# Kernel tuning notes

Measured on AMD Instinct MI355X. Metric: run time of the kernel, lower is better.

Reference implementation:

```python
import jax, jax.numpy as jnp
import numpy as np

NT, NGRID, NX, H, NY = 365, 512, 256, 1024, 1
DR = 0.5

def setup_inputs() -> dict:
    key = jax.random.key(0)
    ks = jax.random.split(key, 8)
    s = 1.0 / np.sqrt(H)
    x = jax.random.normal(ks[0], (NT, NGRID, NX), dtype=jnp.float32)
    # variational dropout mask on input: Bernoulli(1-dr)/(1-dr), fixed across timesteps
    keep = 1.0 - DR
    maskX = (jax.random.uniform(ks[1], (NGRID, NX)) < keep).astype(jnp.float32) / keep
    W_ih = jax.random.uniform(ks[2], (4 * H, NX), minval=-s, maxval=s, dtype=jnp.float32)
    W_hh = jax.random.uniform(ks[3], (4 * H, H), minval=-s, maxval=s, dtype=jnp.float32)
    b_ih = jax.random.uniform(ks[4], (4 * H,), minval=-s, maxval=s, dtype=jnp.float32)
    b_hh = jax.random.uniform(ks[5], (4 * H,), minval=-s, maxval=s, dtype=jnp.float32)
    W_lin = jax.random.uniform(ks[6], (NY, H), minval=-s, maxval=s, dtype=jnp.float32)
    b_lin = jax.random.uniform(ks[7], (NY,), minval=-s, maxval=s, dtype=jnp.float32)
    return {"x": x, "maskX": maskX, "W_ih": W_ih, "W_hh": W_hh,
            "b_ih": b_ih, "b_hh": b_hh, "W_lin": W_lin, "b_lin": b_lin}

def reference(x, maskX, W_ih, W_hh, b_ih, b_hh, W_lin, b_lin):
    ngrid = x.shape[1]
    hidden = W_hh.shape[1]
    # dropout mask applied to input at every step (maskH is never used in the original forward)
    xm = x * maskX[None, :, :]                       # [nt, ngrid, nx]
    # precompute input-to-gate projections for all timesteps (one big GEMM)
    gx = jnp.einsum('tbn,gn->tbg', xm, W_ih) + b_ih + b_hh  # [nt, ngrid, 4H]

    def step(carry, gxt):
        h, c = carry
        gates = gxt + h @ W_hh.T                     # [ngrid, 4H]
        i, f, g, o = jnp.split(gates, 4, axis=-1)    # PyTorch LSTMCell gate order
        i = jax.nn.sigmoid(i)
        f = jax.nn.sigmoid(f)
        g = jnp.tanh(g)
        o = jax.nn.sigmoid(o)
        c = f * c + i * g
        h = o * jnp.tanh(c)
        return (h, c), h

    h0 = jnp.zeros((ngrid, hidden), dtype=x.dtype)
    c0 = jnp.zeros((ngrid, hidden), dtype=x.dtype)
    _, hs = jax.lax.scan(step, (h0, c0), gx)          # hs: [nt, ngrid, H]
    out = jnp.einsum('tbh,yh->tby', hs, W_lin) + b_lin
    return out
```

## Files before the change

kernel.cpp:

```cpp
#include <hip/hip_runtime.h>
#include <hip/hip_bf16.h>
#include <stdint.h>

#define NT 365
#define NGRID 512
#define NX 256
#define HID 1024

typedef __bf16 bf16x8 __attribute__((ext_vector_type(8)));
typedef float f32x16 __attribute__((ext_vector_type(16)));
typedef float f32x4  __attribute__((ext_vector_type(4)));
typedef int   i32x4  __attribute__((ext_vector_type(4)));

__device__ __forceinline__ unsigned short f2bf(float f) {
    union { float f; uint32_t u; } v; v.f = f;
    uint32_t u = v.u;
    uint32_t r = (u + 0x7FFFu + ((u >> 16) & 1u)) >> 16;
    return (unsigned short)r;
}
__device__ __forceinline__ float sigmoidf_(float x) {
    return 1.0f / (1.0f + __expf(-x));
}
__device__ __forceinline__ float tanhf_(float x) {
    return 1.0f - 2.0f / (__expf(2.0f * x) + 1.0f);
}
__device__ __forceinline__ f32x16 mfma(bf16x8 a, bf16x8 b, f32x16 c) {
    return __builtin_amdgcn_mfma_f32_32x32x16_bf16(a, b, c, 0, 0, 0);
}


__global__ void pack_w_kernel(const float* __restrict__ W_ih,
                              const float* __restrict__ W_hh,
                              unsigned short* __restrict__ WP) {
    int tid = blockIdx.x * blockDim.x + threadIdx.x;
    if (tid >= 128 * 80 * 64) return;
    int l  = tid & 63;
    int kt = (tid >> 6) % 80;
    int jg = tid / (80 * 64);
    int n = l & 31;
    int gate = n & 3;
    int j = jg * 8 + (n >> 2);
    int k = kt * 16 + ((l >> 5) << 3);
    int row = gate * HID + j;
    const float* src = (k < HID) ? (W_hh + (size_t)row * HID + k)
                                 : (W_ih + (size_t)row * NX + (k - HID));
    unsigned short* dst = WP + (size_t)tid * 8;
    #pragma unroll
    for (int e = 0; e < 8; ++e) dst[e] = f2bf(src[e]);
}

__global__ void pack_xm_kernel(const float* __restrict__ x,
                               const float* __restrict__ maskX,
                               unsigned short* __restrict__ XM) {
    size_t tid = (size_t)blockIdx.x * blockDim.x + threadIdx.x;
    if (tid >= (size_t)NT * 16384) return;
    int l  = tid & 63;
    int a  = (tid >> 6) & 1;
    int kt = (tid >> 7) & 15;
    int bi = (tid >> 11) & 7;
    int t  = tid >> 14;
    int b = bi * 64 + a * 32 + (l & 31);
    int n = kt * 16 + ((l >> 5) << 3);
    const float* xs = x + ((size_t)t * NGRID + b) * NX + n;
    const float* ms = maskX + (size_t)b * NX + n;
    unsigned short* dst = XM + tid * 8;
    #pragma unroll
    for (int e = 0; e < 8; ++e) dst[e] = f2bf(xs[e] * ms[e]);
}

__global__ void init_kernel(float* __restrict__ out,
                            const float* __restrict__ b_lin,
                            int* __restrict__ ctr, int prefill) {
    int i = blockIdx.x * blockDim.x + threadIdx.x;
    if (i < 1024) ctr[i] = 0;
    if (prefill && i < NT * NGRID) out[i] = b_lin[0];
}

__global__ void reduce_out_kernel(const float* __restrict__ OPart,
                                  const float* __restrict__ b_lin,
                                  float* __restrict__ out) {
    int i = blockIdx.x * blockDim.x + threadIdx.x;
    if (i >= NT * NGRID) return;
    int t = i >> 9, b = i & 511;
    int bi = b >> 6, bl = b & 63;
    const float* p = OPart + ((size_t)(t * 8 + bi) * 32) * 64 + bl;
    float s = b_lin[0];
    #pragma unroll
    for (int g = 0; g < 32; ++g) s += p[g * 64];
    out[i] = s;
}

template<bool BAL>
__device__ void lstm_loop(int tid, int bi, int wgJ,
                          const unsigned short* __restrict__ WPg,
                          const unsigned short* __restrict__ XMg,
                          unsigned int* __restrict__ hA,
                          unsigned int* __restrict__ hB,
                          const float* __restrict__ b_ih,
                          const float* __restrict__ b_hh,
                          const float* __restrict__ W_lin,
                          float* __restrict__ out,
                          float* __restrict__ OPart,
                          int* __restrict__ flags,
                          i32x4* hsm4)
{
    const int w = tid >> 6;
    const int l = tid & 63;
    const int jg = wgJ * 4 + w;
    const int hk = w & 1;
    const int sA = wgJ * 4 + (w & ~1);

    float* exch = (float*)hsm4;
    float* outred = (float*)hsm4 + 10240;
    unsigned long long* hsm = (unsigned long long*)hsm4;

    const bf16x8* __restrict__ WPvA = (const bf16x8*)WPg + (size_t)sA * 5120
                                      + (size_t)(hk * 32) * 64 + l;
    bf16x8 wregA[32], wregB[32];
    #pragma unroll
    for (int kt = 0; kt < 32; ++kt) {
        wregA[kt] = WPvA[kt * 64];
        wregB[kt] = WPvA[5120 + kt * 64];
    }
    const bf16x8* __restrict__ WPxA = (const bf16x8*)WPg + (size_t)sA * 5120
                                      + (size_t)(64 + hk * 8) * 64 + l;

    const int c = l & 31;
    const int gate = c & 3;
    const int jcol = jg * 8 + (c >> 2);
    const float bias = b_ih[gate * HID + jcol] + b_hh[gate * HID + jcol];

    const int p = l & 3;
    const int rl = l >> 2;
    const float wl0 = W_lin[jg * 8 + 2 * p];
    const float wl1 = W_lin[jg * 8 + 2 * p + 1];

    const bf16x8* __restrict__ XMv = (const bf16x8*)XMg;
    const int voff = tid * 16;

    const uint64_t flags64 = (uint64_t)(uintptr_t)flags;
    const uint64_t sig64   = (uint64_t)(uintptr_t)(flags + wgJ);

    float creg[8];
    #pragma unroll
    for (int k = 0; k < 8; ++k) creg[k] = 0.0f;

    f32x16 aA0, aA1, aB0, aB1;

    auto issue = [&](i32x4* stg, uint64_t base) {
        #pragma unroll
        for (int ch = 0; ch < 8; ++ch)
            asm volatile("global_load_dwordx4 %0, %1, %2 sc0"
                         : "=v"(stg[ch])
                         : "v"(voff), "s"(base + (uint64_t)(ch * 4096)));
    };
    auto lwrite = [&](const i32x4* stg, int reg) {
        #pragma unroll
        for (int ch = 0; ch < 8; ++ch) hsm4[reg * 2048 + ch * 256 + tid] = stg[ch];
    };
    auto mchunk = [&](int reg, int cn) {
        if ((cn >> 1) != hk) return;
        const int kb = (cn & 1) * 16;
        const bf16x8* hls = (const bf16x8*)(hsm4 + reg * 2048);
        #pragma unroll
        for (int kt = 0; kt < 16; ++kt) {
            bf16x8 a0 = hls[kt * 128 + l];
            bf16x8 a1 = hls[kt * 128 + 64 + l];
            aA0 = mfma(a0, wregA[kb + kt], aA0);
            aA1 = mfma(a1, wregA[kb + kt], aA1);
            aB0 = mfma(a0, wregB[kb + kt], aB0);
            aB1 = mfma(a1, wregB[kb + kt], aB1);
        }
    };

    #pragma unroll 1
    for (int t = 0; t < NT; ++t) {
        aA0 = (f32x16){}; aA1 = (f32x16){};
        aB0 = (f32x16){}; aB1 = (f32x16){};

        const bf16x8* __restrict__ xp = XMv + (size_t)t * 16384 + bi * 2048
                                        + (hk * 8) * 128 + l;
        #pragma unroll
        for (int kt = 0; kt < 8; ++kt) {
            bf16x8 x0 = xp[kt * 128];
            bf16x8 x1 = xp[kt * 128 + 64];
            bf16x8 bA = WPxA[kt * 64];
            bf16x8 bB = WPxA[5120 + kt * 64];
            aA0 = mfma(x0, bA, aA0);
            aA1 = mfma(x1, bA, aA1);
            aB0 = mfma(x0, bB, aB0);
            aB1 = mfma(x1, bB, aB1);
        }

        if (t > 0 && tid < 32) {
            if constexpr (BAL) {
                while (true) {
                    int v;
                    asm volatile("global_load_dword %0, %1, %2 sc0\n\t"
                                 "s_waitcnt vmcnt(0)"
                                 : "=v"(v)
                                 : "v"(tid * 4), "s"(flags64)
                                 : "memory");
                    if (v >= t) break;
                }
            } else {
                while (__hip_atomic_load(flags + tid, __ATOMIC_RELAXED,
                                         __HIP_MEMORY_SCOPE_AGENT) < t)
                    __builtin_amdgcn_s_sleep(2);
            }
        }
        __syncthreads();

        if (t > 0) {
            __asm__ volatile("" ::: "memory");
            const char* hb = (const char*)((t & 1) ? hA : hB) + (size_t)bi * 131072;

            if constexpr (BAL) {
                uint64_t hb64 = (uint64_t)(uintptr_t)hb;
                i32x4 s0[8];
                issue(s0, hb64);
                asm volatile("s_waitcnt vmcnt(0)" ::: "memory");
                lwrite(s0, 0);
                issue(s0, hb64 + 32768);
                __syncthreads();
                mchunk(0, 0);
                asm volatile("s_waitcnt vmcnt(0)" ::: "memory");
                lwrite(s0, 1);
                issue(s0, hb64 + 65536);
                __syncthreads();
                mchunk(1, 1);
                asm volatile("s_waitcnt vmcnt(0)" ::: "memory");
                lwrite(s0, 0);
                issue(s0, hb64 + 98304);
                __syncthreads();
                mchunk(0, 2);
                asm volatile("s_waitcnt vmcnt(0)" ::: "memory");
                lwrite(s0, 1);
                __syncthreads();
                mchunk(1, 3);
                __syncthreads();
            } else {
                const unsigned long long* __restrict__ hr =
                    (const unsigned long long*)hb + tid;
                unsigned long long stg[16];
                #pragma unroll
                for (int ch = 0; ch < 16; ++ch)
                    stg[ch] = __hip_atomic_load(hr + ch * 256, __ATOMIC_RELAXED,
                                                __HIP_MEMORY_SCOPE_AGENT);
                #pragma unroll
                for (int ch = 0; ch < 16; ++ch) hsm[ch * 256 + tid] = stg[ch];
                __syncthreads();
                #pragma unroll
                for (int ci = 0; ci < 4; ++ci) {
                    if (ci < 3) {
                        #pragma unroll
                        for (int ch = 0; ch < 16; ++ch)
                            stg[ch] = __hip_atomic_load(hr + (ci + 1) * 4096 + ch * 256,
                                                        __ATOMIC_RELAXED,
                                                        __HIP_MEMORY_SCOPE_AGENT);
                    }
                    mchunk(ci & 1, ci);
                    if (ci < 3) {
                        unsigned long long* __restrict__ dst = hsm + ((ci + 1) & 1) * 4096;
                        #pragma unroll
                        for (int ch = 0; ch < 16; ++ch) dst[ch * 256 + tid] = stg[ch];
                    }
                    __syncthreads();
                }
            }
        }

        f32x16 acc0, acc1;
        {
            f32x4* mg4 = (f32x4*)hsm4;
            const int ps = (w ^ 1) * 512;
            if (hk) {
                #pragma unroll
                for (int q = 0; q < 4; ++q) {
                    f32x4 v0, v1;
                    #pragma unroll
                    for (int e = 0; e < 4; ++e) { v0[e] = aA0[4*q+e]; v1[e] = aA1[4*q+e]; }
                    mg4[ps + q * 64 + l]       = v0;
                    mg4[ps + 256 + q * 64 + l] = v1;
                }
            } else {
                #pragma unroll
                for (int q = 0; q < 4; ++q) {
                    f32x4 v0, v1;
                    #pragma unroll
                    for (int e = 0; e < 4; ++e) { v0[e] = aB0[4*q+e]; v1[e] = aB1[4*q+e]; }
                    mg4[ps + q * 64 + l]       = v0;
                    mg4[ps + 256 + q * 64 + l] = v1;
                }
            }
            __syncthreads();
            const int ms = w * 512;
            if (hk) {
                #pragma unroll
                for (int q = 0; q < 4; ++q) {
                    f32x4 u0 = mg4[ms + q * 64 + l];
                    f32x4 u1 = mg4[ms + 256 + q * 64 + l];
                    #pragma unroll
                    for (int e = 0; e < 4; ++e) { aB0[4*q+e] += u0[e]; aB1[4*q+e] += u1[e]; }
                }
                acc0 = aB0; acc1 = aB1;
            } else {
                #pragma unroll
                for (int q = 0; q < 4; ++q) {
                    f32x4 u0 = mg4[ms + q * 64 + l];
                    f32x4 u1 = mg4[ms + 256 + q * 64 + l];
                    #pragma unroll
                    for (int e = 0; e < 4; ++e) { aA0[4*q+e] += u0[e]; aA1[4*q+e] += u1[e]; }
                }
                acc0 = aA0; acc1 = aA1;
            }
            __syncthreads();
        }

        const int jj = c >> 2;
        const int wb = w * 2560;
        #pragma unroll
        for (int ri = 0; ri < 16; ++ri) {
            int r0 = (ri & 3) + 8 * (ri >> 2) + 4 * (l >> 5);
            exch[wb + (r0 * 8 + jj) * 5 + gate]        = acc0[ri] + bias;
            exch[wb + ((r0 + 32) * 8 + jj) * 5 + gate] = acc1[ri] + bias;
        }

        unsigned int* __restrict__ hw =
            ((t & 1) ? hB : hA) + (size_t)bi * 32768 + (jg >> 1) * 512 + p;
        float pr[4];
        #pragma unroll
        for (int k = 0; k < 4; ++k) {
            int r = rl + 16 * k;
            int f0 = wb + (r * 8 + 2 * p) * 5;
            float ia = sigmoidf_(exch[f0 + 0]);
            float fa = sigmoidf_(exch[f0 + 1]);
            float ga = tanhf_(exch[f0 + 2]);
            float oa = sigmoidf_(exch[f0 + 3]);
            float ib = sigmoidf_(exch[f0 + 5]);
            float fb = sigmoidf_(exch[f0 + 6]);
            float gb = tanhf_(exch[f0 + 7]);
            float ob = sigmoidf_(exch[f0 + 8]);
            float c0 = fa * creg[2 * k] + ia * ga;     creg[2 * k] = c0;
            float c1 = fb * creg[2 * k + 1] + ib * gb; creg[2 * k + 1] = c1;
            float h0 = oa * tanhf_(c0);
            float h1 = ob * tanhf_(c1);
            unsigned int pk = (unsigned int)f2bf(h0) | ((unsigned int)f2bf(h1) << 16);
            int a = r >> 5;
            int flane = ((jg & 1) << 5) | (r & 31);
            if constexpr (BAL)
                hw[a * 256 + flane * 4] = pk;
            else
                __hip_atomic_store(&hw[a * 256 + flane * 4], pk, __ATOMIC_RELAXED,
                                   __HIP_MEMORY_SCOPE_AGENT);
            pr[k] = h0 * wl0 + h1 * wl1;
        }

        asm volatile("s_waitcnt vmcnt(0)" ::: "memory");
        __syncthreads();
        if (tid == 0) {
            if constexpr (BAL)
                asm volatile("global_store_dword %0, %1, %2 sc0"
                             :: "v"(0), "v"(t + 1), "s"(sig64) : "memory");
            else
                __hip_atomic_store(flags + wgJ, t + 1, __ATOMIC_RELAXED,
                                   __HIP_MEMORY_SCOPE_AGENT);
        }

        #pragma unroll
        for (int k = 0; k < 4; ++k) {
            float v = pr[k];
            v += __shfl_xor(v, 1);
            v += __shfl_xor(v, 2);
            if (p == 0) outred[w * 64 + rl + 16 * k] = v;
        }
        __syncthreads();
        if (tid < 64) {
            float s = outred[tid] + outred[64 + tid] + outred[128 + tid] + outred[192 + tid];
            if (OPart)
                OPart[((size_t)(t * 8 + bi) * 32 + wgJ) * 64 + tid] = s;
            else
                atomicAdd(out + (size_t)t * NGRID + bi * 64 + tid, s);
        }
    }
}

__global__ __launch_bounds__(256, 1)
void lstm_persist_kernel(const unsigned short* __restrict__ WPg,
                         const unsigned short* __restrict__ XMg,
                         unsigned int* __restrict__ hA,
                         unsigned int* __restrict__ hB,
                         const float* __restrict__ b_ih,
                         const float* __restrict__ b_hh,
                         const float* __restrict__ W_lin,
                         float* __restrict__ out,
                         float* __restrict__ OPart,
                         int* __restrict__ ctr)
{
    __shared__ i32x4 hsm4[4096];
    __shared__ int setup_sh[3];
    const int tid = threadIdx.x;

    if (tid == 0) {
        uint32_t xcc;
        asm volatile("s_getreg_b32 %0, hwreg(HW_REG_XCC_ID)" : "=s"(xcc));
        xcc &= 7;
        int slot = __hip_atomic_fetch_add(&ctr[xcc], 1, __ATOMIC_RELAXED,
                                          __HIP_MEMORY_SCOPE_AGENT);
        asm volatile("s_waitcnt vmcnt(0)" ::: "memory");
        __hip_atomic_fetch_add(&ctr[8], 1, __ATOMIC_RELAXED,
                               __HIP_MEMORY_SCOPE_AGENT);
        while (__hip_atomic_load(&ctr[8], __ATOMIC_RELAXED,
                                 __HIP_MEMORY_SCOPE_AGENT) < 256)
            __builtin_amdgcn_s_sleep(1);
        int bal = 1;
        #pragma unroll
        for (int k = 0; k < 8; ++k)
            bal &= (__hip_atomic_load(&ctr[k], __ATOMIC_RELAXED,
                                      __HIP_MEMORY_SCOPE_AGENT) == 32);
        if (bal && slot < 32) {
            setup_sh[0] = 1; setup_sh[1] = (int)xcc; setup_sh[2] = slot;
        } else {
            setup_sh[0] = 0; setup_sh[1] = blockIdx.x & 7; setup_sh[2] = blockIdx.x >> 3;
        }
    }
    __syncthreads();
    const int bal = setup_sh[0];
    const int bi  = setup_sh[1];
    const int wgJ = setup_sh[2];
    int* flags = ctr + 256 + bi * 32;

    if (bal)
        lstm_loop<true>(tid, bi, wgJ, WPg, XMg, hA, hB, b_ih, b_hh, W_lin,
                        out, OPart, flags, hsm4);
    else
        lstm_loop<false>(tid, bi, wgJ, WPg, XMg, hA, hB, b_ih, b_hh, W_lin,
                         out, OPart, flags, hsm4);
}

extern "C" void kernel_launch(void* const* d_in, const int* in_sizes, int n_in,
                              void* d_out, int out_size, void* d_ws, size_t ws_size,
                              hipStream_t stream)
{
    const float* x     = (const float*)d_in[0];
    const float* maskX = (const float*)d_in[1];
    const float* W_ih  = (const float*)d_in[2];
    const float* W_hh  = (const float*)d_in[3];
    const float* b_ih  = (const float*)d_in[4];
    const float* b_hh  = (const float*)d_in[5];
    const float* W_lin = (const float*)d_in[6];
    const float* b_lin = (const float*)d_in[7];
    float* out = (float*)d_out;

    char* ws = (char*)d_ws;
    const size_t WP_B  = 128ull * 80 * 512 * 2;
    const size_t XM_B  = (size_t)NT * 16384 * 8 * 2;
    const size_t H_B   = (size_t)NGRID * HID * 2;
    const size_t CTR_B = 4096;
    const size_t OP_B  = (size_t)NT * 8 * 32 * 64 * 4;

    unsigned short* WP = (unsigned short*)ws;
    unsigned short* XM = (unsigned short*)(ws + WP_B);
    unsigned int* hA   = (unsigned int*)(ws + WP_B + XM_B);
    unsigned int* hB   = (unsigned int*)(ws + WP_B + XM_B + H_B);
    int* ctr           = (int*)(ws + WP_B + XM_B + 2 * H_B);
    float* OPart       = (float*)(ws + WP_B + XM_B + 2 * H_B + CTR_B);

    const size_t need = WP_B + XM_B + 2 * H_B + CTR_B + OP_B;
    const bool use_part = (ws_size >= need);
    if (!use_part) OPart = nullptr;

    init_kernel<<<(NT * NGRID + 255) / 256, 256, 0, stream>>>(out, b_lin, ctr,
                                                              use_part ? 0 : 1);
    pack_w_kernel<<<(128 * 80 * 64 + 255) / 256, 256, 0, stream>>>(W_ih, W_hh, WP);
    size_t nxm = (size_t)NT * 16384;
    pack_xm_kernel<<<(int)((nxm + 255) / 256), 256, 0, stream>>>(x, maskX, XM);

    lstm_persist_kernel<<<256, 256, 0, stream>>>(WP, XM, hA, hB,
                                                 b_ih, b_hh, W_lin, out, OPart, ctr);
    if (use_part)
        reduce_out_kernel<<<(NT * NGRID + 255) / 256, 256, 0, stream>>>(OPart, b_lin, out);
}
```

Before: 4.829 ms.

## Load full hidden state directly into LDS with global_load_lds per step

The per-step h fetch changes from a four-chunk double-buffered register-staged pipeline to a single bulk asynchronous global-to-LDS copy of the whole 128KB hidden-state slice. Dynamic shared memory grows to 128KB so every chunk fits at once. Each wave then runs its two matrix chunks after a single wait and barrier. This removes the VGPR staging and the several barriers per step, but it gives up overlap between loading and MFMA compute. It also relies on the large LDS allocation and on the default coherence of the async load matching the old sc0 loads.

```diff
diff --git a/kernel.cpp b/kernel.cpp
--- a/kernel.cpp
+++ b/kernel.cpp
@@ -136,7 +136,6 @@
     const float wl1 = W_lin[jg * 8 + 2 * p + 1];
 
     const bf16x8* __restrict__ XMv = (const bf16x8*)XMg;
-    const int voff = tid * 16;
 
     const uint64_t flags64 = (uint64_t)(uintptr_t)flags;
     const uint64_t sig64   = (uint64_t)(uintptr_t)(flags + wgJ);
@@ -147,17 +146,6 @@
 
     f32x16 aA0, aA1, aB0, aB1;
 
-    auto issue = [&](i32x4* stg, uint64_t base) {
-        #pragma unroll
-        for (int ch = 0; ch < 8; ++ch)
-            asm volatile("global_load_dwordx4 %0, %1, %2 sc0"
-                         : "=v"(stg[ch])
-                         : "v"(voff), "s"(base + (uint64_t)(ch * 4096)));
-    };
-    auto lwrite = [&](const i32x4* stg, int reg) {
-        #pragma unroll
-        for (int ch = 0; ch < 8; ++ch) hsm4[reg * 2048 + ch * 256 + tid] = stg[ch];
-    };
     auto mchunk = [&](int reg, int cn) {
         if ((cn >> 1) != hk) return;
         const int kb = (cn & 1) * 16;
@@ -216,28 +204,18 @@
             const char* hb = (const char*)((t & 1) ? hA : hB) + (size_t)bi * 131072;
 
             if constexpr (BAL) {
-                uint64_t hb64 = (uint64_t)(uintptr_t)hb;
-                i32x4 s0[8];
-                issue(s0, hb64);
+                const char* src = hb + (size_t)w * 32768 + (size_t)l * 16;
+                char* dst = (char*)hsm4 + (size_t)w * 32768 + (size_t)l * 16;
+                #pragma unroll
+                for (int ch = 0; ch < 32; ++ch)
+                    __builtin_amdgcn_global_load_lds(
+                        (const __attribute__((address_space(1))) void*)(src + ch * 1024),
+                        (__attribute__((address_space(3))) void*)(dst + ch * 1024),
+                        16, 0, 1 );
                 asm volatile("s_waitcnt vmcnt(0)" ::: "memory");
-                lwrite(s0, 0);
-                issue(s0, hb64 + 32768);
                 __syncthreads();
-                mchunk(0, 0);
-                asm volatile("s_waitcnt vmcnt(0)" ::: "memory");
-                lwrite(s0, 1);
-                issue(s0, hb64 + 65536);
-                __syncthreads();
-                mchunk(1, 1);
-                asm volatile("s_waitcnt vmcnt(0)" ::: "memory");
-                lwrite(s0, 0);
-                issue(s0, hb64 + 98304);
-                __syncthreads();
-                mchunk(0, 2);
-                asm volatile("s_waitcnt vmcnt(0)" ::: "memory");
-                lwrite(s0, 1);
-                __syncthreads();
-                mchunk(1, 3);
+                mchunk(2 * hk + 0, 2 * hk + 0);
+                mchunk(2 * hk + 1, 2 * hk + 1);
                 __syncthreads();
             } else {
                 const unsigned long long* __restrict__ hr =
@@ -397,7 +375,7 @@
                          float* __restrict__ OPart,
                          int* __restrict__ ctr)
 {
-    __shared__ i32x4 hsm4[4096];
+    extern __shared__ i32x4 hsm4[];
     __shared__ int setup_sh[3];
     const int tid = threadIdx.x;
 
@@ -470,14 +448,17 @@
     const bool use_part = (ws_size >= need);
     if (!use_part) OPart = nullptr;
 
+    (void)hipFuncSetAttribute((const void*)lstm_persist_kernel,
+                              hipFuncAttributeMaxDynamicSharedMemorySize, 131072);
+
     init_kernel<<<(NT * NGRID + 255) / 256, 256, 0, stream>>>(out, b_lin, ctr,
                                                               use_part ? 0 : 1);
     pack_w_kernel<<<(128 * 80 * 64 + 255) / 256, 256, 0, stream>>>(W_ih, W_hh, WP);
     size_t nxm = (size_t)NT * 16384;
     pack_xm_kernel<<<(int)((nxm + 255) / 256), 256, 0, stream>>>(x, maskX, XM);
 
-    lstm_persist_kernel<<<256, 256, 0, stream>>>(WP, XM, hA, hB,
-                                                 b_ih, b_hh, W_lin, out, OPart, ctr);
+    lstm_persist_kernel<<<256, 256, 131072, stream>>>(WP, XM, hA, hB,
+                                                      b_ih, b_hh, W_lin, out, OPart, ctr);
     if (use_part)
         reduce_out_kernel<<<(NT * NGRID + 255) / 256, 256, 0, stream>>>(OPart, b_lin, out);
 }
```

Result: faster. 4.034 ms (-16.5%).
